# Kernel tuning notes

Measured on AMD Instinct MI355X. Metric: run time of the kernel, lower is better.

Reference implementation:

```python
import jax, jax.numpy as jnp
import numpy as np

B, S, D, L = 32, 1024, 768, 12

def setup_inputs() -> dict:
    key = jax.random.key(0)
    ks = jax.random.split(key, 10)
    hidden_states = jax.random.normal(ks[0], (B, S, D), dtype=jnp.float32)
    Wq = jax.random.normal(ks[1], (L, D, D), dtype=jnp.float32) * 0.02
    Wk = jax.random.normal(ks[2], (L, D, D), dtype=jnp.float32) * 0.02
    Wv = jax.random.normal(ks[3], (L, D, D), dtype=jnp.float32) * 0.02
    bq = jnp.zeros((L, D), dtype=jnp.float32)
    bk = jnp.zeros((L, D), dtype=jnp.float32)
    bv = jnp.zeros((L, D), dtype=jnp.float32)
    l_k = jnp.full((L, D), 0.8, dtype=jnp.float32)  # iA3 scales, init 0.8 per source
    l_v = jnp.full((L, D), 0.8, dtype=jnp.float32)
    W_head = jax.random.normal(ks[4], (D, 1), dtype=jnp.float32) * 0.02
    b_head = jnp.zeros((1,), dtype=jnp.float32)
    return {"hidden_states": hidden_states, "Wq": Wq, "bq": bq, "Wk": Wk, "bk": bk,
            "Wv": Wv, "bv": bv, "l_k": l_k, "l_v": l_v, "W_head": W_head, "b_head": b_head}

def reference(hidden_states, Wq, bq, Wk, bk, Wv, bv, l_k, l_v, W_head, b_head):
    scale = 1.0 / jnp.sqrt(jnp.float32(D))

    def layer_step(h, params):
        wq, bq_i, wk, bk_i, wv, bv_i, lk, lv = params
        Q = jnp.einsum('bsd,de->bse', h, wq) + bq_i
        K = (jnp.einsum('bsd,de->bse', h, wk) + bk_i) * lk  # iA3 per-channel scale on K
        V = (jnp.einsum('bsd,de->bse', h, wv) + bv_i) * lv  # iA3 per-channel scale on V
        attn = jax.nn.softmax(jnp.einsum('bqd,bkd->bqk', Q, K) * scale, axis=-1)
        h_new = jnp.einsum('bqk,bkd->bqd', attn, V)  # note: no residual/LN, matches source
        return h_new, None

    h, _ = jax.lax.scan(layer_step, hidden_states, (Wq, bq, Wk, bk, Wv, bv, l_k, l_v))
    pooled = h[:, 0, :]  # CLS token
    out = pooled @ W_head + b_head  # [B, 1]
    return out[:, 0]
```

## Files before the change

kernel.cpp:

```cpp
#include <hip/hip_runtime.h>
#include <hip/hip_fp16.h>
#include <math.h>

#define B_ 32
#define S_ 1024
#define D_ 768
#define L_ 12
#define SD 786432LL
#define SS 1048576LL
#define DD 589824LL
#define LDL 1769472LL

typedef _Float16 half8 __attribute__((ext_vector_type(8)));
typedef float f32x4 __attribute__((ext_vector_type(4)));
typedef unsigned short u16;

#define SW(lr) ((((lr) ^ ((lr) >> 3)) & 7))

#define GLD16(p, o) __builtin_amdgcn_global_load_lds( \
        (const __attribute__((address_space(1))) void*)(p), \
        (__attribute__((address_space(3))) void*)&smem[o], 16, 0, 0)


template<int SWIZ>
__global__ __launch_bounds__(256, 2)
void gemm_qkv_k(const __half* __restrict__ A, const __half* __restrict__ Wt,
                const float* __restrict__ biasC, const float* __restrict__ scaleC,
                float aBias,
                __half* __restrict__ CQ, __half* __restrict__ CK, __half* __restrict__ CVt,
                int nBase, int tilesX, int mPerXcd)
{
    __shared__ __align__(16) u16 smem[36864];
    const int K = 768;

    int mIdx, nxI;
    if (SWIZ) {
        const int flat = blockIdx.x;
        const int xcd = flat & 7;
        const int jj = flat >> 3;
        const int mLocal = jj / tilesX;
        nxI = jj - mLocal * tilesX;
        mIdx = xcd * mPerXcd + mLocal;
    } else {
        mIdx = blockIdx.x / tilesX;
        nxI = blockIdx.x - mIdx * tilesX;
    }
    const int m0 = mIdx * 256;
    const int n0 = nxI * 128;

    const int t = threadIdx.x;
    const int l = t & 63, w = t >> 6;
    const int wm = (w & 1) * 128, wn = (w >> 1) * 64;
    const int q = l >> 4, lr = l & 15;

    const int uA0 = t, uA1 = t + 256, uA2 = t + 512, uA3 = t + 768;
    const int uB0 = t, uB1 = t + 256;
#define MKA(u) (A + (long long)(m0 + ((u) >> 2)) * K + ((((u) & 3) ^ ((((u) >> 2) >> 1) & 3)) * 8))
#define MKB(u) (Wt + (long long)(n0 + ((u) >> 2)) * K + ((((u) & 3) ^ ((((u) >> 2) >> 1) & 3)) * 8))
    const __half* gA0 = MKA(uA0); const __half* gA1 = MKA(uA1);
    const __half* gA2 = MKA(uA2); const __half* gA3 = MKA(uA3);
    const __half* gB0 = MKB(uB0); const __half* gB1 = MKB(uB1);
#undef MKA
#undef MKB

    int aoff[8], boff[4];
    #pragma unroll
    for (int mf = 0; mf < 8; ++mf) {
        int rr = wm + mf * 16 + lr;
        aoff[mf] = (rr * 4 + (q ^ ((rr >> 1) & 3))) * 8;
    }
    #pragma unroll
    for (int nf = 0; nf < 4; ++nf) {
        int rb = wn + nf * 16 + lr;
        boff[nf] = (rb * 4 + (q ^ ((rb >> 1) & 3))) * 8;
    }

    f32x4 acc[8][4];
    #pragma unroll
    for (int i = 0; i < 8; ++i)
        #pragma unroll
        for (int j = 0; j < 4; ++j)
            acc[i][j] = (f32x4){0.f, 0.f, 0.f, 0.f};

    GLD16(gA0, uA0 * 8); GLD16(gA1, uA1 * 8); GLD16(gA2, uA2 * 8); GLD16(gA3, uA3 * 8);
    GLD16(gB0, 8192 + uB0 * 8); GLD16(gB1, 8192 + uB1 * 8);
    GLD16(gA0 + 32, 12288 + uA0 * 8); GLD16(gA1 + 32, 12288 + uA1 * 8);
    GLD16(gA2 + 32, 12288 + uA2 * 8); GLD16(gA3 + 32, 12288 + uA3 * 8);
    GLD16(gB0 + 32, 12288 + 8192 + uB0 * 8); GLD16(gB1 + 32, 12288 + 8192 + uB1 * 8);

    int cur = 0;
    #pragma unroll 3
    for (int k0 = 0; k0 < K; k0 += 32) {
        if (k0 + 32 < K) asm volatile("s_waitcnt vmcnt(6)\n\ts_barrier" ::: "memory");
        else             asm volatile("s_waitcnt vmcnt(0)\n\ts_barrier" ::: "memory");
        if (k0 + 64 < K) {
            const int ts = (cur + 2 >= 3) ? (cur - 1) : (cur + 2);
            const int tb = ts * 12288;
            GLD16(gA0 + k0 + 64, tb + uA0 * 8); GLD16(gA1 + k0 + 64, tb + uA1 * 8);
            GLD16(gA2 + k0 + 64, tb + uA2 * 8); GLD16(gA3 + k0 + 64, tb + uA3 * 8);
            GLD16(gB0 + k0 + 64, tb + 8192 + uB0 * 8);
            GLD16(gB1 + k0 + 64, tb + 8192 + uB1 * 8);
        }
        const int sa = cur * 12288, sb = sa + 8192;
        half8 af[8], bf[4];
        #pragma unroll
        for (int mf = 0; mf < 8; ++mf) af[mf] = *(const half8*)(const void*)&smem[sa + aoff[mf]];
        #pragma unroll
        for (int nf = 0; nf < 4; ++nf) bf[nf] = *(const half8*)(const void*)&smem[sb + boff[nf]];
        #pragma unroll
        for (int nf = 0; nf < 4; ++nf)
            #pragma unroll
            for (int mf = 0; mf < 8; ++mf)
                acc[mf][nf] = __builtin_amdgcn_mfma_f32_16x16x32_f16(af[mf], bf[nf], acc[mf][nf], 0, 0, 0);
        __builtin_amdgcn_sched_barrier(0);
        cur = (cur >= 2) ? 0 : (cur + 1);
    }
    __syncthreads();

    const int nCat0 = n0 + nBase;
    const int region = nCat0 / 768;
    const int colBase = nCat0 - region * 768;

    float badd[4], bmul[4];
    #pragma unroll
    for (int nt = 0; nt < 4; ++nt) {
        int gn = nCat0 + wn + nt * 16 + lr;
        badd[nt] = aBias * biasC[gn];
        bmul[nt] = scaleC[gn];
    }

    #pragma unroll
    for (int mf = 0; mf < 8; ++mf) {
        #pragma unroll
        for (int nt = 0; nt < 4; ++nt) {
            #pragma unroll
            for (int i = 0; i < 4; ++i) {
                int lrow = wm + mf * 16 + q * 4 + i;
                int lcol = wn + nt * 16 + lr;
                float v = (acc[mf][nt][i] + badd[nt]) * bmul[nt];
                int cc = lcol >> 3, c7 = lcol & 7;
                smem[lrow * 128 + ((cc ^ (lrow & 15)) << 3) + c7] =
                    __half_as_ushort(__float2half(v));
            }
        }
    }
    __syncthreads();

    if (region < 2) {
        __half* Creg = region ? CK : CQ;
        #pragma unroll
        for (int p = 0; p < 16; ++p) {
            int u = t + p * 256;
            int R = u >> 4, cc = u & 15;
            half8 val = *(const half8*)(const void*)&smem[R * 128 + ((cc ^ (R & 15)) << 3)];
            *(half8*)(void*)&Creg[(long long)(m0 + R) * 768 + colBase + cc * 8] = val;
        }
    } else {
        long long b = m0 >> 10;
        const int mrow0 = m0 & 1023;
        #pragma unroll
        for (int p = 0; p < 16; ++p) {
            int u = t + p * 256;
            int n = u >> 5, mc = u & 31;
            __align__(16) u16 tmp[8];
            #pragma unroll
            for (int j = 0; j < 8; ++j) {
                int m = mc * 8 + j;
                tmp[j] = smem[m * 128 + ((((n >> 3) ^ (m & 15))) << 3) + (n & 7)];
            }
            __half* dst = CVt + b * SD + (long long)(colBase + n) * 1024 + mrow0 + mc * 8;
            *(half8*)(void*)dst = *(const half8*)(const void*)tmp;
        }
    }
}

template<int SWIZ>
__global__ __launch_bounds__(256, 2)
void gemm_qk_k(const __half* __restrict__ A, const __half* __restrict__ B,
               float aAcc, __half* __restrict__ C, float* __restrict__ rsp,
               int tilesX, int tilesPB, int bpx)
{
    __shared__ __align__(16) u16 smem[36864];
    const int K = 768;

    int nxI, ny;
    long long bz;
    if (SWIZ) {
        int flat = blockIdx.x;
        int xcd = flat & 7;
        int j = flat >> 3;
        int bLocal = j / tilesPB;
        int tt = j - bLocal * tilesPB;
        bz = (long long)(xcd * bpx + bLocal);
        ny = tt / tilesX;
        nxI = tt - ny * tilesX;
    } else {
        nxI = blockIdx.x; ny = blockIdx.y; bz = blockIdx.z;
    }

    const int t = threadIdx.x;
    const int l = t & 63, w = t >> 6;
    const int m0 = ny * 256;
    const int n0 = nxI * 128;
    A += bz * SD; B += bz * SD; C += bz * SS;

    const int wm = (w & 1) * 128, wn = (w >> 1) * 64;
    const int q = l >> 4, lr = l & 15;

    const int uA0 = t, uA1 = t + 256, uA2 = t + 512, uA3 = t + 768;
    const int uB0 = t, uB1 = t + 256;
#define MKA(u) (A + (long long)(m0 + ((u) >> 2)) * K + ((((u) & 3) ^ ((((u) >> 2) >> 1) & 3)) * 8))
#define MKB(u) (B + (long long)(n0 + ((u) >> 2)) * K + ((((u) & 3) ^ ((((u) >> 2) >> 1) & 3)) * 8))
    const __half* gA0 = MKA(uA0); const __half* gA1 = MKA(uA1);
    const __half* gA2 = MKA(uA2); const __half* gA3 = MKA(uA3);
    const __half* gB0 = MKB(uB0); const __half* gB1 = MKB(uB1);
#undef MKA
#undef MKB

    int aoff[8], boff[4];
    #pragma unroll
    for (int mf = 0; mf < 8; ++mf) {
        int rr = wm + mf * 16 + lr;
        aoff[mf] = (rr * 4 + (q ^ ((rr >> 1) & 3))) * 8;
    }
    #pragma unroll
    for (int nf = 0; nf < 4; ++nf) {
        int rb = wn + nf * 16 + lr;
        boff[nf] = (rb * 4 + (q ^ ((rb >> 1) & 3))) * 8;
    }

    f32x4 acc[8][4];
    #pragma unroll
    for (int i = 0; i < 8; ++i)
        #pragma unroll
        for (int j = 0; j < 4; ++j)
            acc[i][j] = (f32x4){0.f, 0.f, 0.f, 0.f};

    GLD16(gA0, uA0 * 8); GLD16(gA1, uA1 * 8); GLD16(gA2, uA2 * 8); GLD16(gA3, uA3 * 8);
    GLD16(gB0, 8192 + uB0 * 8); GLD16(gB1, 8192 + uB1 * 8);
    GLD16(gA0 + 32, 12288 + uA0 * 8); GLD16(gA1 + 32, 12288 + uA1 * 8);
    GLD16(gA2 + 32, 12288 + uA2 * 8); GLD16(gA3 + 32, 12288 + uA3 * 8);
    GLD16(gB0 + 32, 12288 + 8192 + uB0 * 8); GLD16(gB1 + 32, 12288 + 8192 + uB1 * 8);

    int cur = 0;
    #pragma unroll 3
    for (int k0 = 0; k0 < K; k0 += 32) {
        if (k0 + 32 < K) asm volatile("s_waitcnt vmcnt(6)\n\ts_barrier" ::: "memory");
        else             asm volatile("s_waitcnt vmcnt(0)\n\ts_barrier" ::: "memory");
        if (k0 + 64 < K) {
            const int ts = (cur + 2 >= 3) ? (cur - 1) : (cur + 2);
            const int tb = ts * 12288;
            GLD16(gA0 + k0 + 64, tb + uA0 * 8); GLD16(gA1 + k0 + 64, tb + uA1 * 8);
            GLD16(gA2 + k0 + 64, tb + uA2 * 8); GLD16(gA3 + k0 + 64, tb + uA3 * 8);
            GLD16(gB0 + k0 + 64, tb + 8192 + uB0 * 8);
            GLD16(gB1 + k0 + 64, tb + 8192 + uB1 * 8);
        }
        const int sa = cur * 12288, sb = sa + 8192;
        half8 af[8], bf[4];
        #pragma unroll
        for (int mf = 0; mf < 8; ++mf) af[mf] = *(const half8*)(const void*)&smem[sa + aoff[mf]];
        #pragma unroll
        for (int nf = 0; nf < 4; ++nf) bf[nf] = *(const half8*)(const void*)&smem[sb + boff[nf]];
        #pragma unroll
        for (int nf = 0; nf < 4; ++nf)
            #pragma unroll
            for (int mf = 0; mf < 8; ++mf)
                acc[mf][nf] = __builtin_amdgcn_mfma_f32_16x16x32_f16(af[mf], bf[nf], acc[mf][nf], 0, 0, 0);
        __builtin_amdgcn_sched_barrier(0);
        cur = (cur >= 2) ? 0 : (cur + 1);
    }
    __syncthreads();

    #pragma unroll
    for (int mf = 0; mf < 8; ++mf) {
        #pragma unroll
        for (int nt = 0; nt < 4; ++nt) {
            #pragma unroll
            for (int i = 0; i < 4; ++i) {
                int lrow = wm + mf * 16 + q * 4 + i;
                int lcol = wn + nt * 16 + lr;
                float v = __expf(acc[mf][nt][i] * aAcc);
                int cc = lcol >> 3, c7 = lcol & 7;
                smem[lrow * 128 + ((cc ^ (lrow & 15)) << 3) + c7] =
                    __half_as_ushort(__float2half(v));
            }
        }
    }
    __syncthreads();

    #pragma unroll
    for (int p = 0; p < 16; ++p) {
        int u = t + p * 256;
        int R = u >> 4, cc = u & 15;
        half8 val = *(const half8*)(const void*)&smem[R * 128 + ((cc ^ (R & 15)) << 3)];
        *(half8*)(void*)&C[(long long)(m0 + R) * 1024 + n0 + cc * 8] = val;
        float s8 = 0.f;
        #pragma unroll
        for (int j = 0; j < 8; ++j) s8 += (float)val[j];
        s8 += __shfl_xor(s8, 1, 16);
        s8 += __shfl_xor(s8, 2, 16);
        s8 += __shfl_xor(s8, 4, 16);
        s8 += __shfl_xor(s8, 8, 16);
        if ((l & 15) == 0)
            rsp[bz * 8192 + (long long)(m0 + R) * 8 + nxI] = s8;
    }
}

template<int SWIZ>
__global__ __launch_bounds__(256, 3)
void gemm_pv_k(const __half* __restrict__ A, const __half* __restrict__ B,
               float aAcc, __half* __restrict__ C, int K, int ldc,
               long long sA, long long sB, long long sC,
               int tilesX, int tilesPB, int bpx,
               const float* __restrict__ invsum)
{
    __shared__ __align__(16) u16 smem[24576];

    int nxI, ny;
    long long bz;
    if (SWIZ) {
        int flat = blockIdx.x;
        int xcd = flat & 7;
        int j = flat >> 3;
        int bLocal = j / tilesPB;
        int tt = j - bLocal * tilesPB;
        bz = (long long)(xcd * bpx + bLocal);
        ny = tt / tilesX;
        nxI = tt - ny * tilesX;
    } else {
        nxI = blockIdx.x; ny = blockIdx.y; bz = blockIdx.z;
    }

    const int t = threadIdx.x;
    const int l = t & 63, w = t >> 6;
    const int n0 = nxI * 128;
    const int m0 = ny * 128;
    A += bz * sA; B += bz * sB; C += bz * sC;

    const int wm = (w & 1) * 64, wn = (w >> 1) * 64;

    const int u0 = t, u1 = t + 256;
    const int r0 = u0 >> 2, c0 = (u0 & 3) ^ ((r0 >> 1) & 3);
    const int r1 = u1 >> 2, c1 = (u1 & 3) ^ ((r1 >> 1) & 3);
    const __half* gA0 = A + (long long)(m0 + r0) * K + c0 * 8;
    const __half* gA1 = A + (long long)(m0 + r1) * K + c1 * 8;
    const __half* gB0 = B + (long long)(n0 + r0) * K + c0 * 8;
    const __half* gB1 = B + (long long)(n0 + r1) * K + c1 * 8;

    int aoff[4], boff[4];
    const int kc = l >> 4;
    #pragma unroll
    for (int mt = 0; mt < 4; ++mt) {
        int rr = wm + mt * 16 + (l & 15);
        aoff[mt] = (rr * 4 + (kc ^ ((rr >> 1) & 3))) * 8;
        int rb = wn + mt * 16 + (l & 15);
        boff[mt] = (rb * 4 + (kc ^ ((rb >> 1) & 3))) * 8;
    }

    f32x4 acc[4][4];
    #pragma unroll
    for (int i = 0; i < 4; ++i)
        #pragma unroll
        for (int j = 0; j < 4; ++j)
            acc[i][j] = (f32x4){0.f, 0.f, 0.f, 0.f};

    GLD16(gA0,      u0 * 8);                 GLD16(gA1,      u1 * 8);
    GLD16(gB0,      12288 + u0 * 8);         GLD16(gB1,      12288 + u1 * 8);
    GLD16(gA0 + 32, 4096 + u0 * 8);          GLD16(gA1 + 32, 4096 + u1 * 8);
    GLD16(gB0 + 32, 12288 + 4096 + u0 * 8);  GLD16(gB1 + 32, 12288 + 4096 + u1 * 8);

    int cur = 0;
    #pragma unroll 3
    for (int k0 = 0; k0 < K; k0 += 32) {
        if (k0 + 32 < K) asm volatile("s_waitcnt vmcnt(4)\n\ts_barrier" ::: "memory");
        else             asm volatile("s_waitcnt vmcnt(0)\n\ts_barrier" ::: "memory");
        if (k0 + 64 < K) {
            const int ts = (cur + 2 >= 3) ? (cur - 1) : (cur + 2);
            const int tsa = ts * 4096, tsb = 12288 + ts * 4096;
            GLD16(gA0 + k0 + 64, tsa + u0 * 8);  GLD16(gA1 + k0 + 64, tsa + u1 * 8);
            GLD16(gB0 + k0 + 64, tsb + u0 * 8);  GLD16(gB1 + k0 + 64, tsb + u1 * 8);
        }
        const int sa = cur * 4096, sb = 12288 + cur * 4096;
        half8 af[4], bf[4];
        #pragma unroll
        for (int mt = 0; mt < 4; ++mt) af[mt] = *(const half8*)(const void*)&smem[sa + aoff[mt]];
        #pragma unroll
        for (int nt = 0; nt < 4; ++nt) bf[nt] = *(const half8*)(const void*)&smem[sb + boff[nt]];
        #pragma unroll
        for (int nt = 0; nt < 4; ++nt)
            #pragma unroll
            for (int mt = 0; mt < 4; ++mt)
                acc[mt][nt] = __builtin_amdgcn_mfma_f32_16x16x32_f16(af[mt], bf[nt], acc[mt][nt], 0, 0, 0);
        __builtin_amdgcn_sched_barrier(0);
        cur = (cur >= 2) ? 0 : (cur + 1);
    }
    __syncthreads();

    float invr[4][4];
    #pragma unroll
    for (int mt = 0; mt < 4; ++mt)
        #pragma unroll
        for (int i = 0; i < 4; ++i)
            invr[mt][i] = invsum[bz * 1024 + m0 + wm + mt * 16 + ((l >> 4) << 2) + i];

    const int qbase = w * 4096;
    #pragma unroll
    for (int mt = 0; mt < 4; ++mt) {
        #pragma unroll
        for (int nt = 0; nt < 4; ++nt) {
            #pragma unroll
            for (int i = 0; i < 4; ++i) {
                int lrow = mt * 16 + ((l >> 4) << 2) + i;
                int lcol = nt * 16 + (l & 15);
                float v = acc[mt][nt][i] * aAcc * invr[mt][i];
                int cc = lcol >> 3, c7 = lcol & 7;
                smem[qbase + lrow * 64 + ((cc ^ SW(lrow)) << 3) + c7] =
                    __half_as_ushort(__float2half(v));
            }
        }
    }
    __syncthreads();

    #pragma unroll
    for (int p = 0; p < 8; ++p) {
        int u = t + p * 256;
        int R = u >> 4, cc = u & 15;
        int qb = ((R >> 6) + ((cc >> 3) << 1)) * 4096;
        int lr2 = R & 63, lcc = cc & 7;
        half8 val = *(const half8*)(const void*)&smem[qb + lr2 * 64 + ((lcc ^ SW(lr2)) << 3)];
        *(half8*)(void*)&C[(long long)(m0 + R) * ldc + n0 + cc * 8] = val;
    }
}

__global__ __launch_bounds__(256)
void rowsuminv_k(const float* __restrict__ rsp, float* __restrict__ inv, int n)
{
    int i = blockIdx.x * 256 + threadIdx.x;
    if (i < n) {
        const float* p = rsp + (long long)i * 8;
        float s = ((p[0] + p[1]) + (p[2] + p[3])) + ((p[4] + p[5]) + (p[6] + p[7]));
        inv[i] = 1.0f / s;
    }
}

__global__ __launch_bounds__(256)
void cvt32to16_k(const float* __restrict__ X, __half* __restrict__ Y)
{
    long long i = ((long long)blockIdx.x * 256 + threadIdx.x) * 4;
    float4 v = *(const float4*)&X[i];
    *(__half2*)&Y[i]     = __floats2half2_rn(v.x, v.y);
    *(__half2*)&Y[i + 2] = __floats2half2_rn(v.z, v.w);
}

__global__ __launch_bounds__(256)
void wtrans_k(const float* __restrict__ W, __half* __restrict__ Wt,
              long long ldL, int rowOff)
{
    __shared__ float Ls[64][65];
    const int lyr = blockIdx.z;
    const int k0 = blockIdx.y * 64, n0 = blockIdx.x * 64;
    const float* src = W + (long long)lyr * DD;
    __half* dst = Wt + (long long)lyr * ldL;
    const int t = threadIdx.x;
    #pragma unroll
    for (int p = 0; p < 4; ++p) {
        int u = t + p * 256;
        int r = u >> 4, c4 = (u & 15) * 4;
        float4 v = *(const float4*)&src[(long long)(k0 + r) * D_ + n0 + c4];
        Ls[r][c4] = v.x; Ls[r][c4 + 1] = v.y; Ls[r][c4 + 2] = v.z; Ls[r][c4 + 3] = v.w;
    }
    __syncthreads();
    #pragma unroll
    for (int p = 0; p < 2; ++p) {
        int u = t + p * 256;
        int n = u >> 3, kc8 = (u & 7) * 8;
        __align__(16) u16 tmp[8];
        #pragma unroll
        for (int j = 0; j < 8; ++j) {
            _Float16 h = (_Float16)Ls[kc8 + j][n];
            tmp[j] = *(const u16*)&h;
        }
        *(half8*)(void*)&dst[(long long)(rowOff + n0 + n) * D_ + k0 + kc8] =
            *(const half8*)(const void*)tmp;
    }
}

__global__ __launch_bounds__(256)
void bscat_k(const float* __restrict__ bq, const float* __restrict__ bk,
             const float* __restrict__ bv, const float* __restrict__ lk,
             const float* __restrict__ lv, float* __restrict__ bsb,
             float* __restrict__ bss)
{
    int i = blockIdx.x * 256 + threadIdx.x;
    if (i >= L_ * 2304) return;
    int l = i / 2304, p = i - l * 2304;
    int r = p / 768, c = p - r * 768;
    float b, s;
    if (r == 0)      { b = bq[l * 768 + c]; s = 1.f; }
    else if (r == 1) { b = bk[l * 768 + c]; s = lk[l * 768 + c]; }
    else             { b = bv[l * 768 + c]; s = lv[l * 768 + c]; }
    bsb[i] = b; bss[i] = s;
}

__global__ __launch_bounds__(256)
void q0_k(const __half* __restrict__ H16, const __half* __restrict__ Wcat,
          const float* __restrict__ bq, float* __restrict__ q0f, float sig)
{
    const int b = blockIdx.x;
    const int n = blockIdx.y * 256 + threadIdx.x;
    const int t = threadIdx.x;
    __shared__ __half hrow[768];
    const __half* h = H16 + (long long)b * SD;
    hrow[t] = h[t]; hrow[t + 256] = h[t + 256]; hrow[t + 512] = h[t + 512];
    __syncthreads();
    const __half* wr = Wcat + 11LL * LDL + (long long)n * 768;
    float acc = 0.f;
    for (int k = 0; k < 768; ++k) acc += (float)hrow[k] * (float)wr[k];
    q0f[b * 768 + n] = acc + sig * bq[11 * 768 + n];
}

__global__ __launch_bounds__(256)
void s0_k(const float* __restrict__ q0f, const __half* __restrict__ K16,
          float* __restrict__ s0f, int b0, float aQK)
{
    const int z = blockIdx.x;
    const int b = b0 + z;
    const int s = blockIdx.y * 256 + threadIdx.x;
    const int t = threadIdx.x;
    __shared__ float qrow[768];
    qrow[t] = q0f[b * 768 + t];
    qrow[t + 256] = q0f[b * 768 + t + 256];
    qrow[t + 512] = q0f[b * 768 + t + 512];
    __syncthreads();
    const __half* kr = K16 + (long long)z * SD + (long long)s * 768;
    float acc = 0.f;
    for (int k = 0; k < 768; ++k) acc += qrow[k] * (float)kr[k];
    s0f[b * 1024 + s] = acc * aQK;
}

__global__ __launch_bounds__(256)
void sm0_k(float* __restrict__ s0f, int b0)
{
    float* p = s0f + (long long)(b0 + blockIdx.x) * 1024;
    const int t = threadIdx.x;
    float v[4];
    float mx = -1e30f;
    #pragma unroll
    for (int j = 0; j < 4; ++j) { v[j] = p[t + 256 * j]; mx = fmaxf(mx, v[j]); }
    __shared__ float red[256];
    red[t] = mx; __syncthreads();
    for (int s = 128; s > 0; s >>= 1) { if (t < s) red[t] = fmaxf(red[t], red[t + s]); __syncthreads(); }
    mx = red[0];
    __syncthreads();
    float sum = 0.f;
    #pragma unroll
    for (int j = 0; j < 4; ++j) { v[j] = __expf(v[j] - mx); sum += v[j]; }
    red[t] = sum; __syncthreads();
    for (int s = 128; s > 0; s >>= 1) { if (t < s) red[t] += red[t + s]; __syncthreads(); }
    const float inv = 1.0f / red[0];
    __syncthreads();
    #pragma unroll
    for (int j = 0; j < 4; ++j) p[t + 256 * j] = v[j] * inv;
}

__global__ __launch_bounds__(256)
void o0_k(const float* __restrict__ p0f, const __half* __restrict__ Vt16,
          float* __restrict__ o0f, int b0, float invSig)
{
    const int z = blockIdx.x;
    const int b = b0 + z;
    const int d = blockIdx.y * 256 + threadIdx.x;
    const int t = threadIdx.x;
    __shared__ float prow[1024];
    #pragma unroll
    for (int j = 0; j < 4; ++j) prow[t + 256 * j] = p0f[b * 1024 + t + 256 * j];
    __syncthreads();
    const __half* vr = Vt16 + (long long)z * SD + (long long)d * 1024;
    float acc = 0.f;
    for (int s = 0; s < 1024; ++s) acc += prow[s] * (float)vr[s];
    o0f[b * 768 + d] = acc * invSig;
}

__global__ __launch_bounds__(256)
void headf_k(const float* __restrict__ o0f, const float* __restrict__ Wh,
             const float* __restrict__ bh, float* __restrict__ out)
{
    const int b = blockIdx.x;
    const int t = threadIdx.x;
    float s = 0.f;
    for (int d = t; d < 768; d += 256) s += o0f[b * 768 + d] * Wh[d];
    __shared__ float red[256];
    red[t] = s; __syncthreads();
    for (int k = 128; k > 0; k >>= 1) { if (t < k) red[t] += red[t + k]; __syncthreads(); }
    if (t == 0) out[b] = red[0] + bh[0];
}

extern "C" void kernel_launch(void* const* d_in, const int* in_sizes, int n_in,
                              void* d_out, int out_size, void* d_ws, size_t ws_size,
                              hipStream_t stream)
{
    const float* hs = (const float*)d_in[0];
    const float* Wq = (const float*)d_in[1];
    const float* bq = (const float*)d_in[2];
    const float* Wk = (const float*)d_in[3];
    const float* bk = (const float*)d_in[4];
    const float* Wv = (const float*)d_in[5];
    const float* bv = (const float*)d_in[6];
    const float* lk = (const float*)d_in[7];
    const float* lv = (const float*)d_in[8];
    const float* Wh = (const float*)d_in[9];
    const float* bh = (const float*)d_in[10];
    float* outp = (float*)d_out;

    __half* H16  = (__half*)d_ws;
    __half* Wcat = H16 + (long long)B_ * SD;
    float*  bsb  = (float*)(Wcat + 12LL * LDL);
    float*  bss  = bsb + 12 * 2304;
    float*  q0f  = bss + 12 * 2304;
    float*  s0f  = q0f + 32 * 768;
    float*  o0f  = s0f + 32 * 1024;
    float*  rsp  = o0f + 32 * 768;
    float*  inv  = rsp + 32LL * 8192;
    __half* Q16  = (__half*)(inv + 32 * 1024);

    const size_t baseBytes = (size_t)((char*)Q16 - (char*)d_ws);
    const size_t perG = ((size_t)(3 * SD) + (size_t)SS) * 2;
    long long avail = (long long)ws_size - (long long)baseBytes;
    int G = (avail > 0) ? (int)(avail / perG) : 1;
    if (G >= 32) G = 32; else if (G >= 16) G = 16; else if (G >= 8) G = 8;
    if (G < 1) G = 1;
    __half* K16  = Q16 + (long long)G * SD;
    __half* Vt16 = K16 + (long long)G * SD;
    __half* P16  = Vt16 + (long long)G * SD;

    cvt32to16_k<<<dim3((int)((B_ * SD) / 1024)), 256, 0, stream>>>(hs, H16);
    wtrans_k<<<dim3(12, 12, 12), 256, 0, stream>>>(Wq, Wcat, LDL, 0);
    wtrans_k<<<dim3(12, 12, 12), 256, 0, stream>>>(Wk, Wcat, LDL, 768);
    wtrans_k<<<dim3(12, 12, 12), 256, 0, stream>>>(Wv, Wcat, LDL, 1536);
    bscat_k<<<dim3((L_ * 2304 + 255) / 256), 256, 0, stream>>>(bq, bk, bv, lk, lv, bsb, bss);

    const float scq = 0.036084391824351615f;
    float sig = 1.f;

    for (int lyr = 0; lyr < L_ - 1; ++lyr) {
        const __half* W = Wcat + (long long)lyr * LDL;
        const float* bb = bsb + lyr * 2304;
        const float* ss = bss + lyr * 2304;
        const float aQK = scq / (sig * sig);

        for (int b0 = 0; b0 < B_; b0 += G) {
            const int nb = (B_ - b0 < G) ? (B_ - b0) : G;
            const __half* hg = H16 + (long long)b0 * SD;

            if ((nb & 1) == 0) {
                gemm_qkv_k<1><<<dim3(8 * (nb >> 1) * 18), 256, 0, stream>>>(
                    hg, W, bb, ss, sig, Q16, K16, Vt16, 0, 18, nb >> 1);
            } else {
                gemm_qkv_k<0><<<dim3(nb * 4 * 18), 256, 0, stream>>>(
                    hg, W, bb, ss, sig, Q16, K16, Vt16, 0, 18, 0);
            }

            if ((nb & 7) == 0) {
                gemm_qk_k<1><<<dim3(nb * 32), 256, 0, stream>>>(
                    Q16, K16, aQK, P16, rsp, 8, 32, nb >> 3);
            } else {
                gemm_qk_k<0><<<dim3(8, 4, nb), 256, 0, stream>>>(
                    Q16, K16, aQK, P16, rsp, 8, 32, 1);
            }

            rowsuminv_k<<<dim3(nb * 4), 256, 0, stream>>>(rsp, inv, nb * 1024);

            if ((nb & 7) == 0) {
                gemm_pv_k<1><<<dim3(nb * 48), 256, 0, stream>>>(
                    P16, Vt16, 4.f, H16 + (long long)b0 * SD, 1024, 768, SS, SD, SD,
                    6, 48, nb >> 3, inv);
            } else {
                gemm_pv_k<0><<<dim3(6, 8, nb), 256, 0, stream>>>(
                    P16, Vt16, 4.f, H16 + (long long)b0 * SD, 1024, 768, SS, SD, SD,
                    6, 48, 1, inv);
            }
        }
        sig *= 4.f;
    }

    const float aQK = scq / (sig * sig);
    q0_k<<<dim3(B_, 3), 256, 0, stream>>>(H16, Wcat, bq, q0f, sig);

    for (int b0 = 0; b0 < B_; b0 += G) {
        const int nb = (B_ - b0 < G) ? (B_ - b0) : G;
        const __half* hg = H16 + (long long)b0 * SD;

        if ((nb & 1) == 0) {
            gemm_qkv_k<1><<<dim3(8 * (nb >> 1) * 12), 256, 0, stream>>>(
                hg, Wcat + 11LL * LDL + 768LL * 768, bsb + 11 * 2304, bss + 11 * 2304,
                sig, K16 , K16, Vt16, 768, 12, nb >> 1);
        } else {
            gemm_qkv_k<0><<<dim3(nb * 4 * 12), 256, 0, stream>>>(
                hg, Wcat + 11LL * LDL + 768LL * 768, bsb + 11 * 2304, bss + 11 * 2304,
                sig, K16 , K16, Vt16, 768, 12, 0);
        }

        s0_k<<<dim3(nb, 4), 256, 0, stream>>>(q0f, K16, s0f, b0, aQK);
        sm0_k<<<dim3(nb), 256, 0, stream>>>(s0f, b0);
        o0_k<<<dim3(nb, 3), 256, 0, stream>>>(s0f, Vt16, o0f, b0, 1.f / sig);
    }

    headf_k<<<dim3(B_), 256, 0, stream>>>(o0f, Wh, bh, outp);
}
```

Before: 3.796 ms.

## Shrink QKV GEMM LDS to double buffer and split epilogue for 3 blocks/CU

```diff
diff --git a/kernel.cpp b/kernel.cpp
--- a/kernel.cpp
+++ b/kernel.cpp
@@ -16,21 +16,21 @@
 typedef unsigned short u16;
 
 #define SW(lr) ((((lr) ^ ((lr) >> 3)) & 7))
+#define KEY16(r) (((r) ^ ((r) >> 3)) & 15)
 
 #define GLD16(p, o) __builtin_amdgcn_global_load_lds( \
         (const __attribute__((address_space(1))) void*)(p), \
         (__attribute__((address_space(3))) void*)&smem[o], 16, 0, 0)
 
-
 template<int SWIZ>
-__global__ __launch_bounds__(256, 2)
+__global__ __launch_bounds__(256, 3)
 void gemm_qkv_k(const __half* __restrict__ A, const __half* __restrict__ Wt,
                 const float* __restrict__ biasC, const float* __restrict__ scaleC,
                 float aBias,
                 __half* __restrict__ CQ, __half* __restrict__ CK, __half* __restrict__ CVt,
                 int nBase, int tilesX, int mPerXcd)
 {
-    __shared__ __align__(16) u16 smem[36864];
+    __shared__ __align__(16) u16 smem[24576];
     const int K = 768;
 
     int mIdx, nxI;
@@ -84,22 +84,17 @@
 
     GLD16(gA0, uA0 * 8); GLD16(gA1, uA1 * 8); GLD16(gA2, uA2 * 8); GLD16(gA3, uA3 * 8);
     GLD16(gB0, 8192 + uB0 * 8); GLD16(gB1, 8192 + uB1 * 8);
-    GLD16(gA0 + 32, 12288 + uA0 * 8); GLD16(gA1 + 32, 12288 + uA1 * 8);
-    GLD16(gA2 + 32, 12288 + uA2 * 8); GLD16(gA3 + 32, 12288 + uA3 * 8);
-    GLD16(gB0 + 32, 12288 + 8192 + uB0 * 8); GLD16(gB1 + 32, 12288 + 8192 + uB1 * 8);
 
     int cur = 0;
-    #pragma unroll 3
+    #pragma unroll 2
     for (int k0 = 0; k0 < K; k0 += 32) {
-        if (k0 + 32 < K) asm volatile("s_waitcnt vmcnt(6)\n\ts_barrier" ::: "memory");
-        else             asm volatile("s_waitcnt vmcnt(0)\n\ts_barrier" ::: "memory");
-        if (k0 + 64 < K) {
-            const int ts = (cur + 2 >= 3) ? (cur - 1) : (cur + 2);
-            const int tb = ts * 12288;
-            GLD16(gA0 + k0 + 64, tb + uA0 * 8); GLD16(gA1 + k0 + 64, tb + uA1 * 8);
-            GLD16(gA2 + k0 + 64, tb + uA2 * 8); GLD16(gA3 + k0 + 64, tb + uA3 * 8);
-            GLD16(gB0 + k0 + 64, tb + 8192 + uB0 * 8);
-            GLD16(gB1 + k0 + 64, tb + 8192 + uB1 * 8);
+        asm volatile("s_waitcnt vmcnt(0)\n\ts_barrier" ::: "memory");
+        if (k0 + 32 < K) {
+            const int tb = (cur ^ 1) * 12288;
+            GLD16(gA0 + k0 + 32, tb + uA0 * 8); GLD16(gA1 + k0 + 32, tb + uA1 * 8);
+            GLD16(gA2 + k0 + 32, tb + uA2 * 8); GLD16(gA3 + k0 + 32, tb + uA3 * 8);
+            GLD16(gB0 + k0 + 32, tb + 8192 + uB0 * 8);
+            GLD16(gB1 + k0 + 32, tb + 8192 + uB1 * 8);
         }
         const int sa = cur * 12288, sb = sa + 8192;
         half8 af[8], bf[4];
@@ -113,7 +108,7 @@
             for (int mf = 0; mf < 8; ++mf)
                 acc[mf][nf] = __builtin_amdgcn_mfma_f32_16x16x32_f16(af[mf], bf[nf], acc[mf][nf], 0, 0, 0);
         __builtin_amdgcn_sched_barrier(0);
-        cur = (cur >= 2) ? 0 : (cur + 1);
+        cur ^= 1;
     }
     __syncthreads();
 
@@ -130,46 +125,51 @@
     }
 
     #pragma unroll
-    for (int mf = 0; mf < 8; ++mf) {
-        #pragma unroll
-        for (int nt = 0; nt < 4; ++nt) {
+    for (int h = 0; h < 2; ++h) {
+        if (h) __syncthreads();
+        if ((w & 1) == h) {
             #pragma unroll
-            for (int i = 0; i < 4; ++i) {
-                int lrow = wm + mf * 16 + q * 4 + i;
-                int lcol = wn + nt * 16 + lr;
-                float v = (acc[mf][nt][i] + badd[nt]) * bmul[nt];
-                int cc = lcol >> 3, c7 = lcol & 7;
-                smem[lrow * 128 + ((cc ^ (lrow & 15)) << 3) + c7] =
-                    __half_as_ushort(__float2half(v));
+            for (int mf = 0; mf < 8; ++mf) {
+                #pragma unroll
+                for (int nt = 0; nt < 4; ++nt) {
+                    #pragma unroll
+                    for (int i = 0; i < 4; ++i) {
+                        int r7 = mf * 16 + q * 4 + i;
+                        int lcol = wn + nt * 16 + lr;
+                        float v = (acc[mf][nt][i] + badd[nt]) * bmul[nt];
+                        int cc = lcol >> 3, c7 = lcol & 7;
+                        smem[r7 * 128 + ((cc ^ KEY16(r7)) << 3) + c7] =
+                            __half_as_ushort(__float2half(v));
+                    }
+                }
             }
         }
-    }
-    __syncthreads();
-
-    if (region < 2) {
-        __half* Creg = region ? CK : CQ;
-        #pragma unroll
-        for (int p = 0; p < 16; ++p) {
-            int u = t + p * 256;
-            int R = u >> 4, cc = u & 15;
-            half8 val = *(const half8*)(const void*)&smem[R * 128 + ((cc ^ (R & 15)) << 3)];
-            *(half8*)(void*)&Creg[(long long)(m0 + R) * 768 + colBase + cc * 8] = val;
-        }
-    } else {
-        long long b = m0 >> 10;
-        const int mrow0 = m0 & 1023;
-        #pragma unroll
-        for (int p = 0; p < 16; ++p) {
-            int u = t + p * 256;
-            int n = u >> 5, mc = u & 31;
-            __align__(16) u16 tmp[8];
+        __syncthreads();
+        if (region < 2) {
+            __half* Creg = region ? CK : CQ;
             #pragma unroll
-            for (int j = 0; j < 8; ++j) {
-                int m = mc * 8 + j;
-                tmp[j] = smem[m * 128 + ((((n >> 3) ^ (m & 15))) << 3) + (n & 7)];
+            for (int p = 0; p < 8; ++p) {
+                int u = t + p * 256;
+                int R = u >> 4, cc = u & 15;
+                half8 val = *(const half8*)(const void*)&smem[R * 128 + ((cc ^ KEY16(R)) << 3)];
+                *(half8*)(void*)&Creg[(long long)(m0 + h * 128 + R) * 768 + colBase + cc * 8] = val;
             }
-            __half* dst = CVt + b * SD + (long long)(colBase + n) * 1024 + mrow0 + mc * 8;
-            *(half8*)(void*)dst = *(const half8*)(const void*)tmp;
+        } else {
+            long long b = m0 >> 10;
+            const int mrow0 = (m0 & 1023) + h * 128;
+            #pragma unroll
+            for (int p = 0; p < 8; ++p) {
+                int u = t + p * 256;
+                int ncol = u >> 4, mcl = u & 15;
+                __align__(16) u16 tmp[8];
+                #pragma unroll
+                for (int j = 0; j < 8; ++j) {
+                    int r7 = mcl * 8 + j;
+                    tmp[j] = smem[r7 * 128 + ((((ncol >> 3) ^ KEY16(r7))) << 3) + (ncol & 7)];
+                }
+                __half* dst = CVt + b * SD + (long long)(colBase + ncol) * 1024 + mrow0 + mcl * 8;
+                *(half8*)(void*)dst = *(const half8*)(const void*)tmp;
+            }
         }
     }
 }
@@ -281,7 +281,7 @@
                 int lcol = wn + nt * 16 + lr;
                 float v = __expf(acc[mf][nt][i] * aAcc);
                 int cc = lcol >> 3, c7 = lcol & 7;
-                smem[lrow * 128 + ((cc ^ (lrow & 15)) << 3) + c7] =
+                smem[lrow * 128 + ((cc ^ KEY16(lrow)) << 3) + c7] =
                     __half_as_ushort(__float2half(v));
             }
         }
@@ -292,7 +292,7 @@
     for (int p = 0; p < 16; ++p) {
         int u = t + p * 256;
         int R = u >> 4, cc = u & 15;
-        half8 val = *(const half8*)(const void*)&smem[R * 128 + ((cc ^ (R & 15)) << 3)];
+        half8 val = *(const half8*)(const void*)&smem[R * 128 + ((cc ^ KEY16(R)) << 3)];
         *(half8*)(void*)&C[(long long)(m0 + R) * 1024 + n0 + cc * 8] = val;
         float s8 = 0.f;
         #pragma unroll
```

Result: slower. 7.815 ms (+105.9%).
